# Kernel optimization log

Hardware: AMD Instinct MI355X
Metric: run time of the kernel (lower is better)

Reference implementation:

```python
import jax, jax.numpy as jnp
import numpy as np

IN_C, HID_C, OUT_C = 128, 256, 128
N_NODES, N_EDGES = 50000, 600000


def setup_inputs() -> dict:
    key = jax.random.key(0)
    ks = jax.random.split(key, 8)
    x = jax.random.normal(ks[0], (N_NODES, IN_C), dtype=jnp.float32)
    edge_index = jax.random.randint(ks[1], (2, N_EDGES), 0, N_NODES, dtype=jnp.int64)
    def glorot(k, shape):
        lim = np.sqrt(6.0 / (shape[0] + shape[1])).astype(np.float32)
        return jax.random.uniform(k, shape, dtype=jnp.float32, minval=-lim, maxval=lim)
    # PyG SAGEConv: out = lin_l(mean_aggr) + lin_r(x_root); bias only in lin_l
    W1_l = glorot(ks[2], (IN_C, HID_C)); b1 = jnp.zeros((HID_C,), jnp.float32)
    W1_r = glorot(ks[3], (IN_C, HID_C))
    W2_l = glorot(ks[4], (HID_C, OUT_C)); b2 = jnp.zeros((OUT_C,), jnp.float32)
    W2_r = glorot(ks[5], (HID_C, OUT_C))
    return {"x": x, "edge_index": edge_index, "W1_l": W1_l, "b1": b1, "W1_r": W1_r,
            "W2_l": W2_l, "b2": b2, "W2_r": W2_r}


def _sage_conv(x, src, dst, W_l, b, W_r):
    n = x.shape[0]
    msg = x[src]  # [E, C] gather from source nodes
    agg = jax.ops.segment_sum(msg, dst, num_segments=n)
    cnt = jax.ops.segment_sum(jnp.ones((src.shape[0],), x.dtype), dst, num_segments=n)
    agg = agg / jnp.maximum(cnt, 1.0)[:, None]  # mean aggregation, zero-deg safe
    return agg @ W_l + b + x @ W_r


def reference(x, edge_index, W1_l, b1, W1_r, W2_l, b2, W2_r):
    src, dst = edge_index[0], edge_index[1]
    h = jax.nn.relu(_sage_conv(x, src, dst, W1_l, b1, W1_r))
    return _sage_conv(h, src, dst, W2_l, b2, W2_r)
```

## Files before the change

### kernel.cpp

```cpp
#include <hip/hip_runtime.h>
#include <hip/hip_bf16.h>


#define N_NODES 50000
#define IN_C    128
#define HID_C   256
#define OUT_C   128
#define N_EDGES 600000

#define PB_CNT  2344
#define PB_W1   (PB_CNT + 256)
#define PB_W2   (PB_W1 + 256)
#define PB_X    (PB_W2 + 6250)

typedef __attribute__((ext_vector_type(8))) short short8;
typedef __attribute__((ext_vector_type(4))) float f32x4;
typedef __attribute__((ext_vector_type(2))) float f32x2;

__device__ __forceinline__ float bf2f(short s) {
    union { unsigned u; float f; } c;
    c.u = ((unsigned)(unsigned short)s) << 16;
    return c.f;
}
__device__ __forceinline__ unsigned f2fp8(float v) {
    return (unsigned)__builtin_amdgcn_cvt_pk_fp8_f32(v, v, 0, false) & 0xffu;
}
__device__ __forceinline__ void acc_fp8x4(float* a, unsigned u) {
    f32x2 lo = __builtin_amdgcn_cvt_pk_f32_fp8(u, false);
    f32x2 hi = __builtin_amdgcn_cvt_pk_f32_fp8(u, true);
    a[0] += lo[0]; a[1] += lo[1]; a[2] += hi[0]; a[3] += hi[1];
}

__global__ __launch_bounds__(256) void prep(
    const float* __restrict__ x, __hip_bfloat16* __restrict__ A1,
    const float* __restrict__ W1l, const float* __restrict__ W1r,
    const float* __restrict__ W2l, const float* __restrict__ W2r,
    __hip_bfloat16* __restrict__ W1t, __hip_bfloat16* __restrict__ W2t,
    const int* __restrict__ dstI, int* __restrict__ cnt) {
    int b = blockIdx.x;
    if (b < PB_CNT) {
        int e = b * 256 + threadIdx.x;
        if (e < N_EDGES) atomicAdd(&cnt[dstI[e]], 1);
    } else if (b < PB_W1) {
        int reg = b - PB_CNT;
        int half = reg >> 7;
        int t = (reg & 127) * 256 + threadIdx.x;
        int k = t >> 8, n = t & 255;
        const float* src = half ? W1r : W1l;
        W1t[n * 256 + half * 128 + k] = __float2bfloat16(src[t]);
    } else if (b < PB_W2) {
        int reg = b - PB_W1;
        int half = reg >> 7;
        int t = (reg & 127) * 256 + threadIdx.x;
        int k = t >> 7, n = t & 127;
        const float* src = half ? W2r : W2l;
        W2t[(size_t)(half * 128 + n) * 256 + k] = __float2bfloat16(src[t]);
    } else {
        int t = (b - PB_W2) * 256 + threadIdx.x;
        if (t >= N_NODES * 32) return;
        int row = t >> 5, c = (t & 31) * 4;
        float4 v = *(const float4*)(x + (size_t)row * 128 + c);
        __hip_bfloat16* d = A1 + (size_t)row * 256 + 128 + c;
        __hip_bfloat162 p0, p1;
        p0.x = __float2bfloat16(v.x); p0.y = __float2bfloat16(v.y);
        p1.x = __float2bfloat16(v.z); p1.y = __float2bfloat16(v.w);
        *(__hip_bfloat162*)d = p0;
        *(__hip_bfloat162*)(d + 2) = p1;
    }
}

__global__ __launch_bounds__(256) void assign_offsets(
    const int* __restrict__ cnt, int* __restrict__ row_ptr,
    int* __restrict__ cursor, int* __restrict__ total, int n) {
    __shared__ int tmp[256];
    __shared__ int sbase;
    int t = threadIdx.x, g = blockIdx.x * 256 + t;
    int v = (g < n) ? cnt[g] : 0;
    tmp[t] = v; __syncthreads();
    for (int off = 1; off < 256; off <<= 1) {
        int u = (t >= off) ? tmp[t - off] : 0;
        __syncthreads();
        tmp[t] += u;
        __syncthreads();
    }
    if (t == 255) sbase = atomicAdd(total, tmp[255]);
    __syncthreads();
    if (g < n) {
        int e = sbase + tmp[t] - v;
        row_ptr[g] = e;
        cursor[g] = e;
    }
}

__global__ void fill_csr(const int* __restrict__ srcI, const int* __restrict__ dstI,
                         int* __restrict__ cursor, int* __restrict__ col, int E) {
    int e = blockIdx.x * blockDim.x + threadIdx.x;
    if (e < E) {
        int pos = atomicAdd(&cursor[dstI[e]], 1);
        col[pos] = srcI[e];
    }
}

__global__ __launch_bounds__(256) void aggregate_bf16(
    const __hip_bfloat16* __restrict__ feat, int featStride,
    const int* __restrict__ row_ptr, const int* __restrict__ deg,
    const int* __restrict__ col,
    __hip_bfloat16* __restrict__ outp, int outStride, int nNodes) {
    int node = blockIdx.x * 16 + (threadIdx.x >> 4);
    int sl   = threadIdx.x & 15;
    if (node >= nNodes) return;
    int beg = row_ptr[node];
    int d   = deg[node];
    const __hip_bfloat16* base = feat + sl * 8;
    float a[8];
    #pragma unroll
    for (int c = 0; c < 8; ++c) a[c] = 0.f;

    short8 v0, v1, v2, v3;
    int j = 0;
    if (d >= 4) {
        int s0 = col[beg + 0], s1 = col[beg + 1];
        int s2 = col[beg + 2], s3 = col[beg + 3];
        v0 = *(const short8*)(base + (size_t)s0 * featStride);
        v1 = *(const short8*)(base + (size_t)s1 * featStride);
        v2 = *(const short8*)(base + (size_t)s2 * featStride);
        v3 = *(const short8*)(base + (size_t)s3 * featStride);
        for (; j + 8 <= d; j += 4) {
            int t0 = col[beg + j + 4], t1 = col[beg + j + 5];
            int t2 = col[beg + j + 6], t3 = col[beg + j + 7];
            short8 w0 = *(const short8*)(base + (size_t)t0 * featStride);
            short8 w1 = *(const short8*)(base + (size_t)t1 * featStride);
            short8 w2 = *(const short8*)(base + (size_t)t2 * featStride);
            short8 w3 = *(const short8*)(base + (size_t)t3 * featStride);
            #pragma unroll
            for (int c = 0; c < 8; ++c)
                a[c] += (bf2f(v0[c]) + bf2f(v1[c])) + (bf2f(v2[c]) + bf2f(v3[c]));
            v0 = w0; v1 = w1; v2 = w2; v3 = w3;
        }
        #pragma unroll
        for (int c = 0; c < 8; ++c)
            a[c] += (bf2f(v0[c]) + bf2f(v1[c])) + (bf2f(v2[c]) + bf2f(v3[c]));
        j += 4;
    }
    int rem = d - j;
    if (rem > 0) {
        int s0 = col[beg + j];
        int s1 = (rem > 1) ? col[beg + j + 1] : s0;
        int s2 = (rem > 2) ? col[beg + j + 2] : s0;
        short8 t0 = *(const short8*)(base + (size_t)s0 * featStride);
        short8 t1 = *(const short8*)(base + (size_t)s1 * featStride);
        short8 t2 = *(const short8*)(base + (size_t)s2 * featStride);
        #pragma unroll
        for (int c = 0; c < 8; ++c) a[c] += bf2f(t0[c]);
        if (rem > 1) {
            #pragma unroll
            for (int c = 0; c < 8; ++c) a[c] += bf2f(t1[c]);
        }
        if (rem > 2) {
            #pragma unroll
            for (int c = 0; c < 8; ++c) a[c] += bf2f(t2[c]);
        }
    }

    float inv = 1.f / (float)max(d, 1);
    __hip_bfloat16* o = outp + (size_t)node * outStride + sl * 8;
    short8 q;
    #pragma unroll
    for (int c = 0; c < 8; ++c) {
        union { __hip_bfloat16 b; short s; } cv;
        cv.b = __float2bfloat16(a[c] * inv);
        q[c] = cv.s;
    }
    *(short8*)o = q;
}

__global__ __launch_bounds__(256) void aggregate_fp8_final(
    const unsigned char* __restrict__ feat,
    const int* __restrict__ row_ptr, const int* __restrict__ deg,
    const int* __restrict__ col,
    float* __restrict__ outp, const float* __restrict__ pre, int nNodes) {
    int node = blockIdx.x * 16 + (threadIdx.x >> 4);
    int sl   = threadIdx.x & 15;
    if (node >= nNodes) return;
    int beg = row_ptr[node];
    int d   = deg[node];
    const unsigned char* base = feat + sl * 8;
    float a[8];
    #pragma unroll
    for (int c = 0; c < 8; ++c) a[c] = 0.f;

    uint2 v0, v1, v2, v3;
    int j = 0;
    if (d >= 4) {
        int s0 = col[beg + 0], s1 = col[beg + 1];
        int s2 = col[beg + 2], s3 = col[beg + 3];
        v0 = *(const uint2*)(base + (size_t)s0 * 128);
        v1 = *(const uint2*)(base + (size_t)s1 * 128);
        v2 = *(const uint2*)(base + (size_t)s2 * 128);
        v3 = *(const uint2*)(base + (size_t)s3 * 128);
        for (; j + 8 <= d; j += 4) {
            int t0 = col[beg + j + 4], t1 = col[beg + j + 5];
            int t2 = col[beg + j + 6], t3 = col[beg + j + 7];
            uint2 w0 = *(const uint2*)(base + (size_t)t0 * 128);
            uint2 w1 = *(const uint2*)(base + (size_t)t1 * 128);
            uint2 w2 = *(const uint2*)(base + (size_t)t2 * 128);
            uint2 w3 = *(const uint2*)(base + (size_t)t3 * 128);
            acc_fp8x4(a,     v0.x); acc_fp8x4(a,     v1.x);
            acc_fp8x4(a,     v2.x); acc_fp8x4(a,     v3.x);
            acc_fp8x4(a + 4, v0.y); acc_fp8x4(a + 4, v1.y);
            acc_fp8x4(a + 4, v2.y); acc_fp8x4(a + 4, v3.y);
            v0 = w0; v1 = w1; v2 = w2; v3 = w3;
        }
        acc_fp8x4(a,     v0.x); acc_fp8x4(a,     v1.x);
        acc_fp8x4(a,     v2.x); acc_fp8x4(a,     v3.x);
        acc_fp8x4(a + 4, v0.y); acc_fp8x4(a + 4, v1.y);
        acc_fp8x4(a + 4, v2.y); acc_fp8x4(a + 4, v3.y);
        j += 4;
    }
    for (; j < d; ++j) {
        uint2 v = *(const uint2*)(base + (size_t)col[beg + j] * 128);
        acc_fp8x4(a, v.x);
        acc_fp8x4(a + 4, v.y);
    }

    float inv = 1.f / (float)max(d, 1);
    const float* pp = pre + (size_t)node * 128 + sl * 8;
    float* op = outp + (size_t)node * 128 + sl * 8;
    float4 p0 = *(const float4*)pp;
    float4 p1 = *(const float4*)(pp + 4);
    *(float4*)op       = make_float4(a[0] * inv + p0.x, a[1] * inv + p0.y,
                                     a[2] * inv + p0.z, a[3] * inv + p0.w);
    *(float4*)(op + 4) = make_float4(a[4] * inv + p1.x, a[5] * inv + p1.y,
                                     a[6] * inv + p1.z, a[7] * inv + p1.w);
}


#define GBM 128
#define GBN 128
#define GBK 64

__device__ __forceinline__ void gload16(const void* g, void* l) {
    typedef const __attribute__((address_space(1))) unsigned int* gp_t;
    typedef __attribute__((address_space(3))) unsigned int* lp_t;
    __builtin_amdgcn_global_load_lds((gp_t)g, (lp_t)l, 16, 0, 0);
}

__global__ __launch_bounds__(256) void gemm_mfma(
    const __hip_bfloat16* __restrict__ A, int lda,
    const __hip_bfloat16* __restrict__ Bt,
    const float* __restrict__ bias,
    __hip_bfloat16* __restrict__ outBf,
    unsigned char* __restrict__ outF8,
    float* __restrict__ outF,
    int M, int K, int mode) {
    __shared__ __hip_bfloat16 Als[GBM * GBK];
    __shared__ __hip_bfloat16 Bls[GBN * GBK];

    int tid  = threadIdx.x;
    int wave = tid >> 6, lane = tid & 63;
    int wm = wave >> 1, wn = wave & 1;
    int mb = blockIdx.x * GBM, nb = blockIdx.y * GBN;

    int srow_base = wave * 32;
    int lrow = lane >> 3;
    int pch  = lane & 7;

    f32x4 acc[4][4];
    #pragma unroll
    for (int i = 0; i < 4; ++i)
        #pragma unroll
        for (int j = 0; j < 4; ++j)
            acc[i][j] = (f32x4){0.f, 0.f, 0.f, 0.f};

    for (int kt = 0; kt < K; kt += GBK) {
        #pragma unroll
        for (int t = 0; t < 4; ++t) {
            int rloc = srow_base + t * 8 + lrow;
            int lch  = pch ^ (rloc & 7);
            int ga_row = mb + rloc; if (ga_row >= M) ga_row = M - 1;
            const __hip_bfloat16* ga = A + (size_t)ga_row * lda + kt + lch * 8;
            gload16(ga, &Als[(srow_base + t * 8) * GBK]);
            const __hip_bfloat16* gb = Bt + (size_t)(nb + rloc) * K + kt + lch * 8;
            gload16(gb, &Bls[(srow_base + t * 8) * GBK]);
        }
        __syncthreads();

        #pragma unroll
        for (int ks = 0; ks < GBK; ks += 32) {
            int chunkL = (ks >> 3) + (lane >> 4);
            short8 af[4], bf[4];
            #pragma unroll
            for (int i = 0; i < 4; ++i) {
                int row = wm * 64 + i * 16 + (lane & 15);
                int pc  = chunkL ^ (row & 7);
                af[i] = *(const short8*)&Als[row * GBK + pc * 8];
            }
            #pragma unroll
            for (int j = 0; j < 4; ++j) {
                int row = wn * 64 + j * 16 + (lane & 15);
                int pc  = chunkL ^ (row & 7);
                bf[j] = *(const short8*)&Bls[row * GBK + pc * 8];
            }
            #pragma unroll
            for (int i = 0; i < 4; ++i)
                #pragma unroll
                for (int j = 0; j < 4; ++j)
                    acc[i][j] = __builtin_amdgcn_mfma_f32_16x16x32_bf16(
                        af[i], bf[j], acc[i][j], 0, 0, 0);
        }
        __syncthreads();
    }

    int cn[4];
    float bc[4];
    #pragma unroll
    for (int j = 0; j < 4; ++j) {
        cn[j] = wn * 64 + j * 16 + (lane & 15);
        bc[j] = 0.f;
    }
    if (mode == 0) {
        #pragma unroll
        for (int j = 0; j < 4; ++j) bc[j] = bias[nb + cn[j]];
        #pragma unroll
        for (int i = 0; i < 4; ++i)
            #pragma unroll
            for (int r = 0; r < 4; ++r) {
                int row = mb + wm * 64 + i * 16 + (lane >> 4) * 4 + r;
                if (row >= M) continue;
                #pragma unroll
                for (int j = 0; j < 4; ++j) {
                    float v = fmaxf(acc[i][j][r] + bc[j], 0.f);
                    outBf[(size_t)row * 256 + nb + cn[j]] = __float2bfloat16(v);
                }
            }
    } else if (blockIdx.y == 0) {
        #pragma unroll
        for (int i = 0; i < 4; ++i)
            #pragma unroll
            for (int r = 0; r < 4; ++r) {
                int row = mb + wm * 64 + i * 16 + (lane >> 4) * 4 + r;
                if (row >= M) continue;
                #pragma unroll
                for (int j = 0; j < 4; ++j)
                    outF8[(size_t)row * 128 + cn[j]] = (unsigned char)f2fp8(acc[i][j][r]);
            }
    } else {
        #pragma unroll
        for (int j = 0; j < 4; ++j) bc[j] = bias[cn[j]];
        #pragma unroll
        for (int i = 0; i < 4; ++i)
            #pragma unroll
            for (int r = 0; r < 4; ++r) {
                int row = mb + wm * 64 + i * 16 + (lane >> 4) * 4 + r;
                if (row >= M) continue;
                #pragma unroll
                for (int j = 0; j < 4; ++j)
                    outF[(size_t)row * 128 + cn[j]] = acc[i][j][r] + bc[j];
            }
    }
}

extern "C" void kernel_launch(void* const* d_in, const int* in_sizes, int n_in,
                              void* d_out, int out_size, void* d_ws, size_t ws_size,
                              hipStream_t stream) {
    const float* x    = (const float*)d_in[0];
    const int*   ei   = (const int*)d_in[1];
    const float* W1l  = (const float*)d_in[2];
    const float* b1   = (const float*)d_in[3];
    const float* W1r  = (const float*)d_in[4];
    const float* W2l  = (const float*)d_in[5];
    const float* b2   = (const float*)d_in[6];
    const float* W2r  = (const float*)d_in[7];
    float* out = (float*)d_out;

    const int E = N_EDGES;
    const int N = N_NODES;
    const int* srcI = ei;
    const int* dstI = ei + E;

    char* w = (char*)d_ws;
    int*            cnt     = (int*)(w + 0);
    int*            total   = (int*)(w + 200000);
    int*            row_ptr = (int*)(w + 204800);
    int*            col     = (int*)(w + 409600);
    __hip_bfloat16* W1t     = (__hip_bfloat16*)(w + 2818048);
    __hip_bfloat16* W2t     = (__hip_bfloat16*)(w + 2949120);
    int*            cursor  = (int*)(w + 3080192);
    __hip_bfloat16* A1      = (__hip_bfloat16*)(w + 3280896);
    __hip_bfloat16* h_bf    = (__hip_bfloat16*)(w + 28880896);
    unsigned char*  hp_f8   = (unsigned char*)(w + 54480896);
    float*          pre     = (float*)(w + 67280896);

    hipMemsetAsync(cnt, 0, 200004, stream);
    prep<<<PB_X, 256, 0, stream>>>(x, A1, W1l, W1r, W2l, W2r, W1t, W2t, dstI, cnt);

    assign_offsets<<<(N + 255) / 256, 256, 0, stream>>>(cnt, row_ptr, cursor, total, N);
    fill_csr<<<(E + 255) / 256, 256, 0, stream>>>(srcI, dstI, cursor, col, E);

    aggregate_bf16<<<(N + 15) / 16, 256, 0, stream>>>(
        A1 + 128, 256, row_ptr, cnt, col, A1, 256, N);
    {
        dim3 grid((N + GBM - 1) / GBM, HID_C / GBN);
        gemm_mfma<<<grid, 256, 0, stream>>>(A1, 256, W1t, b1,
                                            h_bf, nullptr, nullptr, N, 256, 0);
    }

    {
        dim3 grid((N + GBM - 1) / GBM, 2);
        gemm_mfma<<<grid, 256, 0, stream>>>(h_bf, 256, W2t, b2,
                                            nullptr, hp_f8, pre, N, 256, 1);
    }
    aggregate_fp8_final<<<(N + 15) / 16, 256, 0, stream>>>(
        hp_f8, row_ptr, cnt, col, out, pre, N);
}
```

Baseline: 234.6 us.

## Use one wave per node in aggregations and stage GEMM epilogue through LDS

Both aggregation kernels now assign a full 64-lane wave to each node, with four 16-lane slots covering different edges at once, then combine the partial sums with cross-lane shuffles. This raises memory-level parallelism for the irregular gathers, at the cost of idle lanes on low-degree nodes and an extra reduction step. The GEMM epilogue for the bf16 and fp8 outputs now writes tiles into shared memory first and then stores them to global memory with coalesced 16-byte writes, replacing scattered scalar stores. That adds a barrier and LDS traffic.

```diff
diff --git a/kernel.cpp b/kernel.cpp
--- a/kernel.cpp
+++ b/kernel.cpp
@@ -106,9 +106,10 @@
     const int* __restrict__ row_ptr, const int* __restrict__ deg,
     const int* __restrict__ col,
     __hip_bfloat16* __restrict__ outp, int outStride, int nNodes) {
-    int node = blockIdx.x * 16 + (threadIdx.x >> 4);
-    int sl   = threadIdx.x & 15;
+    int node = (blockIdx.x * 256 + threadIdx.x) >> 6;
     if (node >= nNodes) return;
+    int lane = threadIdx.x & 63;
+    int slot = lane >> 4, sl = lane & 15;
     int beg = row_ptr[node];
     int d   = deg[node];
     const __hip_bfloat16* base = feat + sl * 8;
@@ -116,62 +117,43 @@
     #pragma unroll
     for (int c = 0; c < 8; ++c) a[c] = 0.f;
 
-    short8 v0, v1, v2, v3;
-    int j = 0;
-    if (d >= 4) {
-        int s0 = col[beg + 0], s1 = col[beg + 1];
-        int s2 = col[beg + 2], s3 = col[beg + 3];
-        v0 = *(const short8*)(base + (size_t)s0 * featStride);
-        v1 = *(const short8*)(base + (size_t)s1 * featStride);
-        v2 = *(const short8*)(base + (size_t)s2 * featStride);
-        v3 = *(const short8*)(base + (size_t)s3 * featStride);
-        for (; j + 8 <= d; j += 4) {
-            int t0 = col[beg + j + 4], t1 = col[beg + j + 5];
-            int t2 = col[beg + j + 6], t3 = col[beg + j + 7];
-            short8 w0 = *(const short8*)(base + (size_t)t0 * featStride);
-            short8 w1 = *(const short8*)(base + (size_t)t1 * featStride);
-            short8 w2 = *(const short8*)(base + (size_t)t2 * featStride);
-            short8 w3 = *(const short8*)(base + (size_t)t3 * featStride);
-            #pragma unroll
-            for (int c = 0; c < 8; ++c)
-                a[c] += (bf2f(v0[c]) + bf2f(v1[c])) + (bf2f(v2[c]) + bf2f(v3[c]));
-            v0 = w0; v1 = w1; v2 = w2; v3 = w3;
-        }
-        #pragma unroll
-        for (int c = 0; c < 8; ++c)
-            a[c] += (bf2f(v0[c]) + bf2f(v1[c])) + (bf2f(v2[c]) + bf2f(v3[c]));
-        j += 4;
-    }
-    int rem = d - j;
-    if (rem > 0) {
-        int s0 = col[beg + j];
-        int s1 = (rem > 1) ? col[beg + j + 1] : s0;
-        int s2 = (rem > 2) ? col[beg + j + 2] : s0;
-        short8 t0 = *(const short8*)(base + (size_t)s0 * featStride);
-        short8 t1 = *(const short8*)(base + (size_t)s1 * featStride);
-        short8 t2 = *(const short8*)(base + (size_t)s2 * featStride);
-        #pragma unroll
-        for (int c = 0; c < 8; ++c) a[c] += bf2f(t0[c]);
-        if (rem > 1) {
-            #pragma unroll
-            for (int c = 0; c < 8; ++c) a[c] += bf2f(t1[c]);
-        }
-        if (rem > 2) {
-            #pragma unroll
-            for (int c = 0; c < 8; ++c) a[c] += bf2f(t2[c]);
-        }
-    }
-
-    float inv = 1.f / (float)max(d, 1);
-    __hip_bfloat16* o = outp + (size_t)node * outStride + sl * 8;
-    short8 q;
+    for (int j = 0; j < d; j += 16) {
+        int e0 = j + slot, e1 = j + 4 + slot, e2 = j + 8 + slot, e3 = j + 12 + slot;
+        int s0 = col[beg + min(e0, d - 1)];
+        int s1 = col[beg + min(e1, d - 1)];
+        int s2 = col[beg + min(e2, d - 1)];
+        int s3 = col[beg + min(e3, d - 1)];
+        short8 v0 = *(const short8*)(base + (size_t)s0 * featStride);
+        short8 v1 = *(const short8*)(base + (size_t)s1 * featStride);
+        short8 v2 = *(const short8*)(base + (size_t)s2 * featStride);
+        short8 v3 = *(const short8*)(base + (size_t)s3 * featStride);
+        bool b0 = e0 < d, b1 = e1 < d, b2 = e2 < d, b3 = e3 < d;
+        #pragma unroll
+        for (int c = 0; c < 8; ++c) {
+            float f0 = b0 ? bf2f(v0[c]) : 0.f;
+            float f1 = b1 ? bf2f(v1[c]) : 0.f;
+            float f2 = b2 ? bf2f(v2[c]) : 0.f;
+            float f3 = b3 ? bf2f(v3[c]) : 0.f;
+            a[c] += (f0 + f1) + (f2 + f3);
+        }
+    }
     #pragma unroll
     for (int c = 0; c < 8; ++c) {
-        union { __hip_bfloat16 b; short s; } cv;
-        cv.b = __float2bfloat16(a[c] * inv);
-        q[c] = cv.s;
-    }
-    *(short8*)o = q;
+        a[c] += __shfl_xor(a[c], 16, 64);
+        a[c] += __shfl_xor(a[c], 32, 64);
+    }
+    if (slot == 0) {
+        float inv = 1.f / (float)max(d, 1);
+        __hip_bfloat16* o = outp + (size_t)node * outStride + sl * 8;
+        short8 q;
+        #pragma unroll
+        for (int c = 0; c < 8; ++c) {
+            union { __hip_bfloat16 b; short s; } cv;
+            cv.b = __float2bfloat16(a[c] * inv);
+            q[c] = cv.s;
+        }
+        *(short8*)o = q;
+    }
 }
 
 __global__ __launch_bounds__(256) void aggregate_fp8_final(
@@ -179,9 +161,10 @@
     const int* __restrict__ row_ptr, const int* __restrict__ deg,
     const int* __restrict__ col,
     float* __restrict__ outp, const float* __restrict__ pre, int nNodes) {
-    int node = blockIdx.x * 16 + (threadIdx.x >> 4);
-    int sl   = threadIdx.x & 15;
+    int node = (blockIdx.x * 256 + threadIdx.x) >> 6;
     if (node >= nNodes) return;
+    int lane = threadIdx.x & 63;
+    int slot = lane >> 4, sl = lane & 15;
     int beg = row_ptr[node];
     int d   = deg[node];
     const unsigned char* base = feat + sl * 8;
@@ -189,49 +172,41 @@
     #pragma unroll
     for (int c = 0; c < 8; ++c) a[c] = 0.f;
 
-    uint2 v0, v1, v2, v3;
-    int j = 0;
-    if (d >= 4) {
-        int s0 = col[beg + 0], s1 = col[beg + 1];
-        int s2 = col[beg + 2], s3 = col[beg + 3];
-        v0 = *(const uint2*)(base + (size_t)s0 * 128);
-        v1 = *(const uint2*)(base + (size_t)s1 * 128);
-        v2 = *(const uint2*)(base + (size_t)s2 * 128);
-        v3 = *(const uint2*)(base + (size_t)s3 * 128);
-        for (; j + 8 <= d; j += 4) {
-            int t0 = col[beg + j + 4], t1 = col[beg + j + 5];
-            int t2 = col[beg + j + 6], t3 = col[beg + j + 7];
-            uint2 w0 = *(const uint2*)(base + (size_t)t0 * 128);
-            uint2 w1 = *(const uint2*)(base + (size_t)t1 * 128);
-            uint2 w2 = *(const uint2*)(base + (size_t)t2 * 128);
-            uint2 w3 = *(const uint2*)(base + (size_t)t3 * 128);
-            acc_fp8x4(a,     v0.x); acc_fp8x4(a,     v1.x);
-            acc_fp8x4(a,     v2.x); acc_fp8x4(a,     v3.x);
-            acc_fp8x4(a + 4, v0.y); acc_fp8x4(a + 4, v1.y);
-            acc_fp8x4(a + 4, v2.y); acc_fp8x4(a + 4, v3.y);
-            v0 = w0; v1 = w1; v2 = w2; v3 = w3;
-        }
+    for (int j = 0; j < d; j += 16) {
+        int e0 = j + slot, e1 = j + 4 + slot, e2 = j + 8 + slot, e3 = j + 12 + slot;
+        int s0 = col[beg + min(e0, d - 1)];
+        int s1 = col[beg + min(e1, d - 1)];
+        int s2 = col[beg + min(e2, d - 1)];
+        int s3 = col[beg + min(e3, d - 1)];
+        uint2 v0 = *(const uint2*)(base + (size_t)s0 * 128);
+        uint2 v1 = *(const uint2*)(base + (size_t)s1 * 128);
+        uint2 v2 = *(const uint2*)(base + (size_t)s2 * 128);
+        uint2 v3 = *(const uint2*)(base + (size_t)s3 * 128);
+        if (e0 >= d) { v0.x = 0u; v0.y = 0u; }
+        if (e1 >= d) { v1.x = 0u; v1.y = 0u; }
+        if (e2 >= d) { v2.x = 0u; v2.y = 0u; }
+        if (e3 >= d) { v3.x = 0u; v3.y = 0u; }
         acc_fp8x4(a,     v0.x); acc_fp8x4(a,     v1.x);
         acc_fp8x4(a,     v2.x); acc_fp8x4(a,     v3.x);
         acc_fp8x4(a + 4, v0.y); acc_fp8x4(a + 4, v1.y);
         acc_fp8x4(a + 4, v2.y); acc_fp8x4(a + 4, v3.y);
-        j += 4;
-    }
-    for (; j < d; ++j) {
-        uint2 v = *(const uint2*)(base + (size_t)col[beg + j] * 128);
-        acc_fp8x4(a, v.x);
-        acc_fp8x4(a + 4, v.y);
-    }
-
-    float inv = 1.f / (float)max(d, 1);
-    const float* pp = pre + (size_t)node * 128 + sl * 8;
-    float* op = outp + (size_t)node * 128 + sl * 8;
-    float4 p0 = *(const float4*)pp;
-    float4 p1 = *(const float4*)(pp + 4);
-    *(float4*)op       = make_float4(a[0] * inv + p0.x, a[1] * inv + p0.y,
-                                     a[2] * inv + p0.z, a[3] * inv + p0.w);
-    *(float4*)(op + 4) = make_float4(a[4] * inv + p1.x, a[5] * inv + p1.y,
-                                     a[6] * inv + p1.z, a[7] * inv + p1.w);
+    }
+    #pragma unroll
+    for (int c = 0; c < 8; ++c) {
+        a[c] += __shfl_xor(a[c], 16, 64);
+        a[c] += __shfl_xor(a[c], 32, 64);
+    }
+    if (slot == 0) {
+        float inv = 1.f / (float)max(d, 1);
+        const float* pp = pre + (size_t)node * 128 + sl * 8;
+        float* op = outp + (size_t)node * 128 + sl * 8;
+        float4 p0 = *(const float4*)pp;
+        float4 p1 = *(const float4*)(pp + 4);
+        *(float4*)op       = make_float4(a[0] * inv + p0.x, a[1] * inv + p0.y,
+                                         a[2] * inv + p0.z, a[3] * inv + p0.w);
+        *(float4*)(op + 4) = make_float4(a[4] * inv + p1.x, a[5] * inv + p1.y,
+                                         a[6] * inv + p1.z, a[7] * inv + p1.w);
+    }
 }
 
 
@@ -253,8 +228,9 @@
     unsigned char* __restrict__ outF8,
     float* __restrict__ outF,
     int M, int K, int mode) {
-    __shared__ __hip_bfloat16 Als[GBM * GBK];
-    __shared__ __hip_bfloat16 Bls[GBN * GBK];
+    __shared__ __hip_bfloat16 sBuf[GBM * GBK * 2];
+    __hip_bfloat16* Als = sBuf;
+    __hip_bfloat16* Bls = sBuf + GBM * GBK;
 
     int tid  = threadIdx.x;
     int wave = tid >> 6, lane = tid & 63;
@@ -325,25 +301,46 @@
         for (int i = 0; i < 4; ++i)
             #pragma unroll
             for (int r = 0; r < 4; ++r) {
-                int row = mb + wm * 64 + i * 16 + (lane >> 4) * 4 + r;
-                if (row >= M) continue;
+                int lr = wm * 64 + i * 16 + (lane >> 4) * 4 + r;
                 #pragma unroll
                 for (int j = 0; j < 4; ++j) {
                     float v = fmaxf(acc[i][j][r] + bc[j], 0.f);
-                    outBf[(size_t)row * 256 + nb + cn[j]] = __float2bfloat16(v);
+                    sBuf[lr * 128 + cn[j]] = __float2bfloat16(v);
                 }
             }
+        __syncthreads();
+        #pragma unroll
+        for (int it = 0; it < 8; ++it) {
+            int chunk = it * 256 + tid;
+            int lr  = chunk >> 4;
+            int lcB = (chunk & 15) * 16;
+            int grow = mb + lr;
+            if (grow < M)
+                *(float4*)((char*)outBf + (size_t)grow * 512 + nb * 2 + lcB) =
+                    *(const float4*)((const char*)sBuf + lr * 256 + lcB);
+        }
     } else if (blockIdx.y == 0) {
+        unsigned char* s8 = (unsigned char*)sBuf;
         #pragma unroll
         for (int i = 0; i < 4; ++i)
             #pragma unroll
             for (int r = 0; r < 4; ++r) {
-                int row = mb + wm * 64 + i * 16 + (lane >> 4) * 4 + r;
-                if (row >= M) continue;
+                int lr = wm * 64 + i * 16 + (lane >> 4) * 4 + r;
                 #pragma unroll
                 for (int j = 0; j < 4; ++j)
-                    outF8[(size_t)row * 128 + cn[j]] = (unsigned char)f2fp8(acc[i][j][r]);
+                    s8[lr * 128 + cn[j]] = (unsigned char)f2fp8(acc[i][j][r]);
             }
+        __syncthreads();
+        #pragma unroll
+        for (int it = 0; it < 4; ++it) {
+            int chunk = it * 256 + tid;
+            int lr  = chunk >> 3;
+            int lcB = (chunk & 7) * 16;
+            int grow = mb + lr;
+            if (grow < M)
+                *(float4*)(outF8 + (size_t)grow * 128 + lcB) =
+                    *(const float4*)(s8 + lr * 128 + lcB);
+        }
     } else {
         #pragma unroll
         for (int j = 0; j < 4; ++j) bc[j] = bias[cn[j]];
@@ -397,7 +394,7 @@
     assign_offsets<<<(N + 255) / 256, 256, 0, stream>>>(cnt, row_ptr, cursor, total, N);
     fill_csr<<<(E + 255) / 256, 256, 0, stream>>>(srcI, dstI, cursor, col, E);
 
-    aggregate_bf16<<<(N + 15) / 16, 256, 0, stream>>>(
+    aggregate_bf16<<<(N + 3) / 4, 256, 0, stream>>>(
         A1 + 128, 256, row_ptr, cnt, col, A1, 256, N);
     {
         dim3 grid((N + GBM - 1) / GBM, HID_C / GBN);
@@ -410,6 +407,6 @@
         gemm_mfma<<<grid, 256, 0, stream>>>(h_bf, 256, W2t, b2,
                                             nullptr, hp_f8, pre, N, 256, 1);
     }
-    aggregate_fp8_final<<<(N + 15) / 16, 256, 0, stream>>>(
+    aggregate_fp8_final<<<(N + 3) / 4, 256, 0, stream>>>(
         hp_f8, row_ptr, cnt, col, out, pre, N);
 }
```

Measured after the change: 241.4 us. 1.03x slower.
